# Kernel tuning notes

Hardware: AMD Instinct MI355X
Metric: run time of the kernel (lower is better)

The kernel has to match this reference:

```python
import jax, jax.numpy as jnp
import numpy as np

B, N, DIN, DH, H_MLP, L, C = 64, 1024, 64, 128, 128, 3, 4


def setup_inputs() -> dict:
    key = jax.random.key(0)
    ks = jax.random.split(key, 12)
    s = 0.05  # weight scale for numerical stability
    return {
        "x": jax.random.normal(ks[0], (B, N, DIN), jnp.float32),
        "U": jax.random.normal(ks[1], (3, N, N), jnp.float32) / np.sqrt(N),
        "w1_0": jax.random.normal(ks[2], (3, DIN, H_MLP), jnp.float32) * s,
        "b1_0": jnp.zeros((3, H_MLP), jnp.float32),
        "w2_0": jax.random.normal(ks[3], (3, H_MLP, DH), jnp.float32) * s,
        "b2_0": jnp.zeros((3, DH), jnp.float32),
        "w1_r": jax.random.normal(ks[4], (L - 1, 3, DH, H_MLP), jnp.float32) * s,
        "b1_r": jnp.zeros((L - 1, 3, H_MLP), jnp.float32),
        "w2_r": jax.random.normal(ks[5], (L - 1, 3, H_MLP, DH), jnp.float32) * s,
        "b2_r": jnp.zeros((L - 1, 3, DH), jnp.float32),
        "bw": jnp.ones((L, 3), jnp.float32),  # weight1/2/3 init to 1.0 per layer
        "Wc1": jax.random.normal(ks[6], (DH, 128), jnp.float32) * s,
        "bc1": jnp.zeros((128,), jnp.float32),
        "alpha": jnp.full((128,), 0.25, jnp.float32),  # PReLU init
        "Wc2": jax.random.normal(ks[7], (128, C), jnp.float32) * s,
        "bc2": jnp.zeros((C,), jnp.float32),
    }


def _gcn_multi(h, U, w1, b1, w2, b2, w3):
    """One GraphConv_multi layer: 3 spectral branches, softmax-weighted sum.
    h: [B,N,D_in], U: [3,N,N], w1:[3,Din,H], w2:[3,H,Dout], w3:[3]."""
    # agg = U^T @ h per branch (U is shared across batch; no repeat needed)
    agg = jnp.einsum('kji,bjd->kbid', U, h)                     # [3,B,N,Din]
    m = jax.nn.relu(jnp.einsum('kbid,kdh->kbih', agg, w1) + b1[:, None, None, :])
    m = jnp.einsum('kbih,kho->kbio', m, w2) + b2[:, None, None, :]  # [3,B,N,Dout]
    out = jnp.einsum('kij,kbjd->kbid', U, m)                    # U @ mlp_out
    ws = jax.nn.softmax(w3)                                     # branch mix
    return jnp.einsum('k,kbid->bid', ws, out)


def reference(x, U, w1_0, b1_0, w2_0, b2_0, w1_r, b1_r, w2_r, b2_r,
              bw, Wc1, bc1, alpha, Wc2, bc2):
    h = jax.nn.relu(_gcn_multi(x, U, w1_0, b1_0, w2_0, b2_0, bw[0]))
    for l in range(w1_r.shape[0]):  # remaining num_layers-1 GCN layers
        h = jax.nn.relu(_gcn_multi(h, U, w1_r[l], b1_r[l], w2_r[l], b2_r[l], bw[l + 1]))
    pooled = jnp.mean(h, axis=1)                                # 'mean' graph pooling
    z = pooled @ Wc1 + bc1
    z = jnp.where(z > 0, z, alpha * z)                          # PReLU(128); dropout = eval no-op
    return z @ Wc2 + bc2                                        # [B, C]
```

## Files before the change

### kernel.cpp

```cpp
#include <hip/hip_runtime.h>


typedef unsigned short u16;
typedef short bf16x8 __attribute__((ext_vector_type(8)));
typedef float f32x4 __attribute__((ext_vector_type(4)));
typedef u16 u16x4 __attribute__((ext_vector_type(4)));

__device__ __forceinline__ u16 f2bf(float x){
  unsigned u = __builtin_bit_cast(unsigned, x);
  u += 0x7fffu + ((u >> 16) & 1u);
  return (u16)(u >> 16);
}
__device__ __forceinline__ float bf2f(u16 h){
  return __builtin_bit_cast(float, ((unsigned)h) << 16);
}
__device__ __forceinline__ void gload16(const u16* g, u16* l){
  __builtin_amdgcn_global_load_lds(
      (const __attribute__((address_space(1))) unsigned int*)(g),
      (__attribute__((address_space(3))) unsigned int*)(l), 16, 0, 0);
}


__global__ void prep_weights(const float* __restrict__ w1_0, const float* __restrict__ w2_0,
                             const float* __restrict__ w1_r, const float* __restrict__ w2_r,
                             const float* __restrict__ bw,
                             u16* __restrict__ W1T0, u16* __restrict__ W2T0,
                             u16* __restrict__ W1Tr, u16* __restrict__ W2Tr,
                             float* __restrict__ wsb){
  int id = blockIdx.x*256 + threadIdx.x;
  if (id < 3){
    float a0=bw[id*3+0], a1=bw[id*3+1], a2=bw[id*3+2];
    float m = fmaxf(a0,fmaxf(a1,a2));
    float e0=expf(a0-m), e1=expf(a1-m), e2=expf(a2-m);
    float s = e0+e1+e2;
    wsb[id*3+0]=e0/s; wsb[id*3+1]=e1/s; wsb[id*3+2]=e2/s;
  }
  if (id < 24576){
    int k=id/8192, rem=id%8192, h=rem/64, d=rem%64;
    W1T0[id] = f2bf(w1_0[(k*64+d)*128 + h]);
  } else if (id < 73728){
    int t=id-24576, k=t/16384, rem=t%16384, o=rem/128, h=rem%128;
    W2T0[t] = f2bf(w2_0[(k*128+h)*128 + o]);
  } else if (id < 172032){
    int t=id-73728, lk=t/16384, rem=t%16384, h=rem/128, d=rem%128;
    W1Tr[t] = f2bf(w1_r[lk*16384 + d*128 + h]);
  } else if (id < 270336){
    int t=id-172032, lk=t/16384, rem=t%16384, o=rem/128, h=rem%128;
    W2Tr[t] = f2bf(w2_r[lk*16384 + h*128 + o]);
  }
}

__global__ void prep_U(const float* __restrict__ U, u16* __restrict__ UTcat,
                       u16* __restrict__ Ucat){
  __shared__ float t[32][33];
  int k = blockIdx.z, i0 = blockIdx.x*32, j0 = blockIdx.y*32;
  size_t kb = (size_t)k << 20;
  #pragma unroll
  for (int rr=0; rr<4; rr++){
    int r = threadIdx.y*4+rr, c = threadIdx.x;
    float v = U[kb + (size_t)(j0+r)*1024 + i0+c];
    t[r][c] = v;
    Ucat[(size_t)(j0+r)*3072 + k*1024 + i0+c] = f2bf(v);
  }
  __syncthreads();
  #pragma unroll
  for (int rr=0; rr<4; rr++){
    int r = threadIdx.y*4+rr, c = threadIdx.x;
    UTcat[kb + (size_t)(i0+r)*1024 + j0+c] = f2bf(t[c][r]);
  }
}

__global__ void prep_x(const float* __restrict__ x, u16* __restrict__ H){
  __shared__ float t[32][33];
  int b = blockIdx.z, d0 = blockIdx.x*32, j0 = blockIdx.y*32;
  #pragma unroll
  for (int rr=0;rr<4;rr++){
    int r=threadIdx.y*4+rr, c=threadIdx.x;
    t[r][c] = x[((size_t)b*1024 + j0+r)*64 + d0+c];
  }
  __syncthreads();
  #pragma unroll
  for (int rr=0;rr<4;rr++){
    int r=threadIdx.y*4+rr, c=threadIdx.x;
    H[(size_t)(b*64 + d0+r)*1024 + j0+c] = f2bf(t[c][r]);
  }
}

template<bool RELU, int REORD>
__global__ __launch_bounds__(512, 4)
void gemm_big(const u16* __restrict__ A, const u16* __restrict__ B,
              u16* __restrict__ C, int Nc, int K, long aZ, int cRowZ)
{
  __shared__ __align__(16) u16 ldsA[3*8192];
  __shared__ __align__(16) u16 ldsB[3*4096];
  const int tid = threadIdx.x;
  const int z = blockIdx.z;
  const u16* Ab = A + (size_t)z*aZ;
  const int gx = gridDim.x;
  const int nwg = gx*gridDim.y;
  int flat = blockIdx.y*gx + blockIdx.x;
  if ((nwg & 7) == 0) flat = (flat & 7)*(nwg >> 3) + (flat >> 3);
  const int bm = (flat/gx)*256, bn = (flat%gx)*128;
  const int wave = tid>>6, lane = tid&63;
  const int wm = (wave&3)*64, wn = (wave>>2)*64;
  const int rl = lane&15, ksb = lane>>4;
  const int srow = tid>>2;
  const int scol = ((tid&3)*8) ^ (((tid>>3)&3)<<3);
  const int NT = K>>5;

  f32x4 acc[4][4];
  #pragma unroll
  for (int mi=0;mi<4;mi++)
    #pragma unroll
    for (int ni=0;ni<4;ni++){ f32x4 zv={0.f,0.f,0.f,0.f}; acc[mi][ni]=zv; }

  auto stage = [&](int t){
    const int sa = (t%3)*8192, sb = (t%3)*4096;
    const int k0 = t<<5;
    #pragma unroll
    for (int c=0;c<2;c++)
      gload16(Ab + (size_t)(bm + c*128 + srow)*K + k0 + scol,
              &ldsA[sa + c*4096 + tid*8]);
    gload16(B + (size_t)(bn + srow)*K + k0 + scol, &ldsB[sb + tid*8]);
  };

  stage(0); stage(1);
  asm volatile("s_waitcnt vmcnt(3)" ::: "memory");
  __builtin_amdgcn_s_barrier();
  __builtin_amdgcn_sched_barrier(0);

  for (int t=0; t<NT; t++){
    const int sa = (t%3)*8192, sb = (t%3)*4096;
    bf16x8 af[4], bfr[4];
    #pragma unroll
    for (int mi=0;mi<4;mi++){
      const int row = wm + mi*16 + rl;
      af[mi] = *(const bf16x8*)&ldsA[sa + row*32 + ((ksb*8) ^ (((row>>1)&3)<<3))];
    }
    #pragma unroll
    for (int ni=0;ni<4;ni++){
      const int row = wn + ni*16 + rl;
      bfr[ni] = *(const bf16x8*)&ldsB[sb + row*32 + ((ksb*8) ^ (((row>>1)&3)<<3))];
    }
    if (t+2 < NT) stage(t+2);
    __builtin_amdgcn_s_setprio(1);
    #pragma unroll
    for (int ni=0;ni<4;ni++)
      #pragma unroll
      for (int mi=0;mi<4;mi++)
        acc[mi][ni] = __builtin_amdgcn_mfma_f32_16x16x32_bf16(af[mi], bfr[ni], acc[mi][ni], 0,0,0);
    __builtin_amdgcn_s_setprio(0);
    if (t+2 < NT)      asm volatile("s_waitcnt vmcnt(3)" ::: "memory");
    else if (t+1 < NT) asm volatile("s_waitcnt vmcnt(0)" ::: "memory");
    __builtin_amdgcn_s_barrier();
    __builtin_amdgcn_sched_barrier(0);
  }

  #pragma unroll
  for (int ni=0;ni<4;ni++){
    const int col = bn + wn + ni*16 + rl;
    #pragma unroll
    for (int mi=0;mi<4;mi++){
      const int row0 = bm + wm + mi*16 + ksb*4;
      #pragma unroll
      for (int r=0;r<4;r++){
        float v = acc[mi][ni][r];
        if (RELU) v = fmaxf(v, 0.f);
        if constexpr (REORD){
          const int Din = 1 << REORD;
          const int bb = col >> REORD, d = col & (Din-1);
          C[((size_t)((z<<6) + bb)*1024 + row0 + r)*Din + d] = f2bf(v);
        } else {
          C[(size_t)(z*cRowZ + row0 + r)*Nc + col] = f2bf(v);
        }
      }
    }
  }
}

__global__ __launch_bounds__(512, 2)
void gemm_agg_mlp(const u16* __restrict__ A, const u16* __restrict__ B,
                  const u16* __restrict__ W1T, const u16* __restrict__ W2T,
                  const float* __restrict__ b1g, const float* __restrict__ b2g,
                  const float* __restrict__ wsl, u16* __restrict__ M2T)
{
  __shared__ __align__(16) u16 lds[69632];
  const int tid = threadIdx.x;
  const int z = blockIdx.z;
  const int K = 1024, NT = 32;
  const u16* Ab = A + (size_t)z*1048576;
  const u16* W1k = W1T + z*16384;
  const u16* W2k = W2T + z*16384;
  const int gx = gridDim.x;
  const int nwg = gx*gridDim.y;
  int flat = blockIdx.y*gx + blockIdx.x;
  if ((nwg & 7) == 0) flat = (flat & 7)*(nwg >> 3) + (flat >> 3);
  const int bm = (flat/gx)*256, bn = (flat%gx)*128;
  const int b = bn >> 7;
  const int wave = tid>>6, lane = tid&63;
  const int wm = (wave&3)*64, wn = (wave>>2)*64;
  const int rl = lane&15, ksb = lane>>4;
  const int xr = (rl&7)<<3;
  const int srow = tid>>2;
  const int scol = ((tid&3)*8) ^ (((tid>>3)&3)<<3);

  f32x4 acc[4][4];
  #pragma unroll
  for (int mi=0;mi<4;mi++)
    #pragma unroll
    for (int ni=0;ni<4;ni++){ f32x4 zv={0.f,0.f,0.f,0.f}; acc[mi][ni]=zv; }

  #pragma unroll
  for (int c=0;c<4;c++){
    const int e = c*4096 + tid*8, row = e>>7, col = e&127;
    gload16(W1k + row*128 + (col ^ ((row&7)<<3)), &lds[36864 + e]);
  }
  #pragma unroll
  for (int c=0;c<4;c++){
    const int e = c*4096 + tid*8, row = e>>7, col = e&127;
    gload16(W2k + row*128 + (col ^ ((row&7)<<3)), &lds[53248 + e]);
  }

  auto stage = [&](int t){
    const int sa = (t%3)*8192, sb = 24576 + (t%3)*4096;
    const int k0 = t<<5;
    #pragma unroll
    for (int c=0;c<2;c++)
      gload16(Ab + (size_t)(bm + c*128 + srow)*K + k0 + scol,
              &lds[sa + c*4096 + tid*8]);
    gload16(B + (size_t)(bn + srow)*K + k0 + scol, &lds[sb + tid*8]);
  };

  stage(0); stage(1);
  asm volatile("s_waitcnt vmcnt(3)" ::: "memory");
  __builtin_amdgcn_s_barrier();
  __builtin_amdgcn_sched_barrier(0);

  for (int t=0; t<NT; t++){
    const int sa = (t%3)*8192, sb = 24576 + (t%3)*4096;
    bf16x8 af[4], bfr[4];
    #pragma unroll
    for (int mi=0;mi<4;mi++){
      const int row = wm + mi*16 + rl;
      af[mi] = *(const bf16x8*)&lds[sa + row*32 + ((ksb*8) ^ (((row>>1)&3)<<3))];
    }
    #pragma unroll
    for (int ni=0;ni<4;ni++){
      const int row = wn + ni*16 + rl;
      bfr[ni] = *(const bf16x8*)&lds[sb + row*32 + ((ksb*8) ^ (((row>>1)&3)<<3))];
    }
    if (t+2 < NT) stage(t+2);
    __builtin_amdgcn_s_setprio(1);
    #pragma unroll
    for (int ni=0;ni<4;ni++)
      #pragma unroll
      for (int mi=0;mi<4;mi++)
        acc[mi][ni] = __builtin_amdgcn_mfma_f32_16x16x32_bf16(af[mi], bfr[ni], acc[mi][ni], 0,0,0);
    __builtin_amdgcn_s_setprio(0);
    if (t+2 < NT)      asm volatile("s_waitcnt vmcnt(3)" ::: "memory");
    else if (t+1 < NT) asm volatile("s_waitcnt vmcnt(0)" ::: "memory");
    __builtin_amdgcn_s_barrier();
    __builtin_amdgcn_sched_barrier(0);
  }

  __syncthreads();
  #pragma unroll
  for (int ni=0;ni<4;ni++){
    const int d = wn + ni*16 + rl;
    #pragma unroll
    for (int mi=0;mi<4;mi++){
      #pragma unroll
      for (int r=0;r<4;r++){
        const int j = wm + mi*16 + ksb*4 + r;
        lds[j*128 + (d ^ ((j&7)<<3))] = f2bf(acc[mi][ni][r]);
      }
    }
  }
  __syncthreads();

  const int jg = (wave&3)*64, hg = (wave>>2)*64;
  f32x4 acc1[4][4];
  #pragma unroll
  for (int mi=0;mi<4;mi++)
    #pragma unroll
    for (int ni=0;ni<4;ni++){ f32x4 zv={0.f,0.f,0.f,0.f}; acc1[mi][ni]=zv; }
  #pragma unroll
  for (int kk=0;kk<4;kk++){
    const int k0 = kk*32;
    bf16x8 aj[4], wh[4];
    #pragma unroll
    for (int mi=0;mi<4;mi++)
      aj[mi] = *(const bf16x8*)&lds[(jg+mi*16+rl)*128 + ((k0+ksb*8) ^ xr)];
    #pragma unroll
    for (int ni=0;ni<4;ni++)
      wh[ni] = *(const bf16x8*)&lds[36864 + (hg+ni*16+rl)*128 + ((k0+ksb*8) ^ xr)];
    #pragma unroll
    for (int ni=0;ni<4;ni++)
      #pragma unroll
      for (int mi=0;mi<4;mi++)
        acc1[mi][ni] = __builtin_amdgcn_mfma_f32_16x16x32_bf16(aj[mi], wh[ni], acc1[mi][ni], 0,0,0);
  }
  __syncthreads();

  float bh[4];
  #pragma unroll
  for (int ni=0;ni<4;ni++) bh[ni] = b1g[z*128 + hg + ni*16 + rl];
  #pragma unroll
  for (int ni=0;ni<4;ni++){
    const int h = hg + ni*16 + rl;
    #pragma unroll
    for (int mi=0;mi<4;mi++){
      #pragma unroll
      for (int r=0;r<4;r++){
        const int j = jg + mi*16 + ksb*4 + r;
        lds[j*128 + (h ^ ((j&7)<<3))] = f2bf(fmaxf(acc1[mi][ni][r] + bh[ni], 0.f));
      }
    }
  }
  __syncthreads();

  const int og = (wave>>2)*64, jg2 = (wave&3)*64;
  f32x4 acc2[4][4];
  #pragma unroll
  for (int mi=0;mi<4;mi++)
    #pragma unroll
    for (int ni=0;ni<4;ni++){ f32x4 zv={0.f,0.f,0.f,0.f}; acc2[mi][ni]=zv; }
  #pragma unroll
  for (int kk=0;kk<4;kk++){
    const int k0 = kk*32;
    bf16x8 wo[4], mj[4];
    #pragma unroll
    for (int mi=0;mi<4;mi++)
      wo[mi] = *(const bf16x8*)&lds[53248 + (og+mi*16+rl)*128 + ((k0+ksb*8) ^ xr)];
    #pragma unroll
    for (int ni=0;ni<4;ni++)
      mj[ni] = *(const bf16x8*)&lds[(jg2+ni*16+rl)*128 + ((k0+ksb*8) ^ xr)];
    #pragma unroll
    for (int ni=0;ni<4;ni++)
      #pragma unroll
      for (int mi=0;mi<4;mi++)
        acc2[mi][ni] = __builtin_amdgcn_mfma_f32_16x16x32_bf16(wo[mi], mj[ni], acc2[mi][ni], 0,0,0);
  }

  const float ws = wsl[z];
  #pragma unroll
  for (int mi=0;mi<4;mi++){
    #pragma unroll
    for (int r=0;r<4;r++){
      const int o = og + mi*16 + ksb*4 + r;
      const float bo = b2g[z*128 + o];
      #pragma unroll
      for (int ni=0;ni<4;ni++){
        const int j = jg2 + ni*16 + rl;
        M2T[(size_t)(b*128 + o)*3072 + z*1024 + bm + j] = f2bf((acc2[mi][ni][r] + bo) * ws);
      }
    }
  }
}

template<int DIN>
__global__ __launch_bounds__(256)
void fused_mlp(const u16* __restrict__ AGG, const u16* __restrict__ W1T,
               const u16* __restrict__ W2T, const float* __restrict__ b1g,
               const float* __restrict__ b2g, const float* __restrict__ wsl,
               u16* __restrict__ M2T)
{
  constexpr int JW1 = 128*DIN;
  __shared__ __align__(16) u16 lds[2*JW1 + 16384];
  const int tid = threadIdx.x;
  const int jt = blockIdx.x, z = blockIdx.z, k = z>>6, b = z&63;
  const u16* Ag  = AGG + ((size_t)z*1024 + jt*128)*DIN;
  const u16* W1k = W1T + k*JW1;
  const u16* W2k = W2T + k*16384;
  const int wave = tid>>6, lane = tid&63;
  const int wm = (wave>>1)*64, wn = (wave&1)*64;
  const int rl = lane&15, ksb = lane>>4;
  const int xr = (rl&7)<<3;

  constexpr int CJ = JW1/2048;
  #pragma unroll
  for (int c=0;c<CJ;c++){
    const int e = c*2048 + tid*8, row = e/DIN, col = e%DIN;
    gload16(Ag + (size_t)row*DIN + (col ^ ((row&7)<<3)), &lds[e]);
  }
  #pragma unroll
  for (int c=0;c<CJ;c++){
    const int e = c*2048 + tid*8, row = e/DIN, col = e%DIN;
    gload16(W1k + (size_t)row*DIN + (col ^ ((row&7)<<3)), &lds[JW1 + e]);
  }
  #pragma unroll
  for (int c=0;c<8;c++){
    const int e = c*2048 + tid*8, row = e>>7, col = e&127;
    gload16(W2k + (size_t)row*128 + (col ^ ((row&7)<<3)), &lds[2*JW1 + e]);
  }
  asm volatile("s_waitcnt vmcnt(8)" ::: "memory");
  __builtin_amdgcn_s_barrier();
  __builtin_amdgcn_sched_barrier(0);

  f32x4 acc[4][4];
  #pragma unroll
  for (int mi=0;mi<4;mi++)
    #pragma unroll
    for (int ni=0;ni<4;ni++){ f32x4 zv={0.f,0.f,0.f,0.f}; acc[mi][ni]=zv; }
  #pragma unroll
  for (int k0=0; k0<DIN; k0+=32){
    bf16x8 aj[4], wh[4];
    #pragma unroll
    for (int mi=0;mi<4;mi++)
      aj[mi] = *(const bf16x8*)&lds[(wm+mi*16+rl)*DIN + ((k0+ksb*8) ^ xr)];
    #pragma unroll
    for (int ni=0;ni<4;ni++)
      wh[ni] = *(const bf16x8*)&lds[JW1 + (wn+ni*16+rl)*DIN + ((k0+ksb*8) ^ xr)];
    #pragma unroll
    for (int ni=0;ni<4;ni++)
      #pragma unroll
      for (int mi=0;mi<4;mi++)
        acc[mi][ni] = __builtin_amdgcn_mfma_f32_16x16x32_bf16(aj[mi], wh[ni], acc[mi][ni], 0,0,0);
  }
  __syncthreads();

  float bh[4];
  #pragma unroll
  for (int ni=0;ni<4;ni++) bh[ni] = b1g[k*128 + wn + ni*16 + rl];
  #pragma unroll
  for (int ni=0;ni<4;ni++){
    const int h = wn + ni*16 + rl;
    #pragma unroll
    for (int mi=0;mi<4;mi++){
      #pragma unroll
      for (int r=0;r<4;r++){
        const int j = wm + mi*16 + ksb*4 + r;
        lds[j*128 + (h ^ ((j&7)<<3))] = f2bf(fmaxf(acc[mi][ni][r] + bh[ni], 0.f));
      }
    }
  }
  __syncthreads();

  f32x4 acc2[4][4];
  #pragma unroll
  for (int mi=0;mi<4;mi++)
    #pragma unroll
    for (int ni=0;ni<4;ni++){ f32x4 zv={0.f,0.f,0.f,0.f}; acc2[mi][ni]=zv; }
  #pragma unroll
  for (int k0=0; k0<128; k0+=32){
    bf16x8 ao[4], mj[4];
    #pragma unroll
    for (int mi=0;mi<4;mi++)
      ao[mi] = *(const bf16x8*)&lds[2*JW1 + (wm+mi*16+rl)*128 + ((k0+ksb*8) ^ xr)];
    #pragma unroll
    for (int ni=0;ni<4;ni++)
      mj[ni] = *(const bf16x8*)&lds[(wn+ni*16+rl)*128 + ((k0+ksb*8) ^ xr)];
    #pragma unroll
    for (int ni=0;ni<4;ni++)
      #pragma unroll
      for (int mi=0;mi<4;mi++)
        acc2[mi][ni] = __builtin_amdgcn_mfma_f32_16x16x32_bf16(ao[mi], mj[ni], acc2[mi][ni], 0,0,0);
  }

  const float ws = wsl[k];
  #pragma unroll
  for (int mi=0;mi<4;mi++){
    #pragma unroll
    for (int r=0;r<4;r++){
      const int o = wm + mi*16 + ksb*4 + r;
      const float bo = b2g[k*128 + o];
      #pragma unroll
      for (int ni=0;ni<4;ni++){
        const int j = wn + ni*16 + rl;
        M2T[(size_t)(b*128 + o)*3072 + k*1024 + jt*128 + j] = f2bf((acc2[mi][ni][r] + bo) * ws);
      }
    }
  }
}

__global__ void pool_kernel(const u16* __restrict__ H, float* __restrict__ pooled){
  const int row = blockIdx.x, t = threadIdx.x;
  u16x4 v = *(const u16x4*)(H + (size_t)row*1024 + t*4);
  float s = bf2f(v.x)+bf2f(v.y)+bf2f(v.z)+bf2f(v.w);
  for (int o2=32;o2>0;o2>>=1) s += __shfl_down(s,o2);
  __shared__ float red[4];
  if ((t&63)==0) red[t>>6]=s;
  __syncthreads();
  if (t==0) pooled[row] = (red[0]+red[1]+red[2]+red[3])*(1.f/1024.f);
}

__global__ void head_kernel(const float* __restrict__ pooled, const float* __restrict__ Wc1,
                            const float* __restrict__ bc1, const float* __restrict__ alpha,
                            const float* __restrict__ Wc2, const float* __restrict__ bc2,
                            float* __restrict__ out){
  const int b = blockIdx.x, h = threadIdx.x;
  __shared__ float p[128], zz[128];
  p[h] = pooled[b*128+h];
  __syncthreads();
  float acc = bc1[h];
  for (int d=0; d<128; d++) acc = fmaf(p[d], Wc1[d*128+h], acc);
  zz[h] = acc>0.f ? acc : alpha[h]*acc;
  __syncthreads();
  if (h<4){
    float a = bc2[h];
    for (int q=0;q<128;q++) a = fmaf(zz[q], Wc2[q*4+h], a);
    out[b*4+h]=a;
  }
}

extern "C" void kernel_launch(void* const* d_in, const int* in_sizes, int n_in,
                              void* d_out, int out_size, void* d_ws, size_t ws_size,
                              hipStream_t stream)
{
  const float* x     = (const float*)d_in[0];
  const float* U     = (const float*)d_in[1];
  const float* w1_0  = (const float*)d_in[2];
  const float* b1_0  = (const float*)d_in[3];
  const float* w2_0  = (const float*)d_in[4];
  const float* b2_0  = (const float*)d_in[5];
  const float* w1_r  = (const float*)d_in[6];
  const float* b1_r  = (const float*)d_in[7];
  const float* w2_r  = (const float*)d_in[8];
  const float* b2_r  = (const float*)d_in[9];
  const float* bw    = (const float*)d_in[10];
  const float* Wc1   = (const float*)d_in[11];
  const float* bc1   = (const float*)d_in[12];
  const float* alpha = (const float*)d_in[13];
  const float* Wc2   = (const float*)d_in[14];
  const float* bc2   = (const float*)d_in[15];
  float* out = (float*)d_out;

  char* wsp = (char*)d_ws;
  size_t off = 0;
  auto alloc = [&](size_t bytes) -> void* {
    void* p = wsp + off;
    off = (off + bytes + 255) & ~(size_t)255;
    return p;
  };
  u16* UTcat = (u16*)alloc(6291456);
  u16* Ucat  = (u16*)alloc(6291456);
  u16* W1T0  = (u16*)alloc(49152);
  u16* W2T0  = (u16*)alloc(98304);
  u16* W1Tr  = (u16*)alloc(196608);
  u16* W2Tr  = (u16*)alloc(196608);
  float* wsb = (float*)alloc(256);
  u16* HT    = (u16*)alloc(16777216);
  u16* AGG   = (u16*)alloc(50331648);
  u16* M2T   = (u16*)alloc(50331648);
  float* pooled = (float*)alloc(32768);
  if (off > ws_size) return;

  prep_weights<<<1056, 256, 0, stream>>>(w1_0,w2_0,w1_r,w2_r,bw,
      W1T0,W2T0,W1Tr,W2Tr,wsb);
  prep_U<<<dim3(32,32,3), dim3(32,8), 0, stream>>>(U, UTcat, Ucat);
  prep_x<<<dim3(2,32,64), dim3(32,8), 0, stream>>>(x, HT);

  for (int l=0; l<3; l++){
    const float* b1 = l ? b1_r + (l-1)*384 : b1_0;
    const float* b2 = l ? b2_r + (l-1)*384 : b2_0;

    if (l == 0){
      gemm_big<false,6><<<dim3(32, 4, 3), 512, 0, stream>>>(
          UTcat, HT, AGG, 4096, 1024, 1048576L, 0);
      fused_mlp<64><<<dim3(8, 1, 192), 256, 0, stream>>>(
          AGG, W1T0, W2T0, b1, b2, wsb, M2T);
    } else {
      gemm_agg_mlp<<<dim3(64, 4, 3), 512, 0, stream>>>(
          UTcat, HT,
          W1Tr + (size_t)(l-1)*3*16384, W2Tr + (size_t)(l-1)*3*16384,
          b1, b2, wsb + l*3, M2T);
    }
    gemm_big<true,0><<<dim3(8, 32, 1), 512, 0, stream>>>(
        M2T, Ucat, HT, 1024, 3072, 0L, 0);
  }
  pool_kernel<<<8192, 256, 0, stream>>>(HT, pooled);
  head_kernel<<<64, 128, 0, stream>>>(pooled, Wc1, bc1, alpha, Wc2, bc2, out);
}
```

Before: 413.0 us.

## Fuse mean pooling into final GEMM epilogue and shrink agg-MLP LDS footprint

The last layer's U@M GEMM now reduces its ReLU outputs per row into partial sums instead of writing the full bf16 activation tensor. A small combine kernel then sums the 16 partials into the pooled vector, which removes a 16 MB write plus reread and the separate pool pass. Separately, gemm_agg_mlp stops staging W1/W2 in LDS and reads them straight from global memory. It processes the MLP in four 64-row chunks, cutting LDS use so launch bounds can request 4 blocks per CU instead of 2. The tradeoff is more global or L2 weight traffic and extra barriers per chunk.

```diff
diff --git a/kernel.cpp b/kernel.cpp
--- a/kernel.cpp
+++ b/kernel.cpp
@@ -86,10 +86,11 @@
   }
 }
 
-template<bool RELU, int REORD>
+template<bool RELU, int REORD, bool POOL>
 __global__ __launch_bounds__(512, 4)
 void gemm_big(const u16* __restrict__ A, const u16* __restrict__ B,
-              u16* __restrict__ C, int Nc, int K, long aZ, int cRowZ)
+              u16* __restrict__ C, float* __restrict__ Pp,
+              int Nc, int K, long aZ, int cRowZ)
 {
   __shared__ __align__(16) u16 ldsA[3*8192];
   __shared__ __align__(16) u16 ldsB[3*4096];
@@ -156,6 +157,26 @@
     __builtin_amdgcn_sched_barrier(0);
   }
 
+  if constexpr (POOL){
+    const int bx = flat % gx;
+    #pragma unroll
+    for (int mi=0;mi<4;mi++){
+      #pragma unroll
+      for (int r=0;r<4;r++){
+        float s = 0.f;
+        #pragma unroll
+        for (int ni=0;ni<4;ni++) s += fmaxf(acc[mi][ni][r], 0.f);
+        s += __shfl_xor(s, 1); s += __shfl_xor(s, 2);
+        s += __shfl_xor(s, 4); s += __shfl_xor(s, 8);
+        if ((lane & 15) == 0){
+          const int row = bm + wm + mi*16 + ksb*4 + r;
+          Pp[(size_t)(bx*2 + (wn>>6))*8192 + row] = s;
+        }
+      }
+    }
+    return;
+  }
+
   #pragma unroll
   for (int ni=0;ni<4;ni++){
     const int col = bn + wn + ni*16 + rl;
@@ -178,13 +199,13 @@
   }
 }
 
-__global__ __launch_bounds__(512, 2)
+__global__ __launch_bounds__(512, 4)
 void gemm_agg_mlp(const u16* __restrict__ A, const u16* __restrict__ B,
                   const u16* __restrict__ W1T, const u16* __restrict__ W2T,
                   const float* __restrict__ b1g, const float* __restrict__ b2g,
                   const float* __restrict__ wsl, u16* __restrict__ M2T)
 {
-  __shared__ __align__(16) u16 lds[69632];
+  __shared__ __align__(16) u16 lds[40960];
   const int tid = threadIdx.x;
   const int z = blockIdx.z;
   const int K = 1024, NT = 32;
@@ -210,17 +231,6 @@
     #pragma unroll
     for (int ni=0;ni<4;ni++){ f32x4 zv={0.f,0.f,0.f,0.f}; acc[mi][ni]=zv; }
 
-  #pragma unroll
-  for (int c=0;c<4;c++){
-    const int e = c*4096 + tid*8, row = e>>7, col = e&127;
-    gload16(W1k + row*128 + (col ^ ((row&7)<<3)), &lds[36864 + e]);
-  }
-  #pragma unroll
-  for (int c=0;c<4;c++){
-    const int e = c*4096 + tid*8, row = e>>7, col = e&127;
-    gload16(W2k + row*128 + (col ^ ((row&7)<<3)), &lds[53248 + e]);
-  }
-
   auto stage = [&](int t){
     const int sa = (t%3)*8192, sb = 24576 + (t%3)*4096;
     const int k0 = t<<5;
@@ -278,83 +288,70 @@
   }
   __syncthreads();
 
-  const int jg = (wave&3)*64, hg = (wave>>2)*64;
-  f32x4 acc1[4][4];
-  #pragma unroll
-  for (int mi=0;mi<4;mi++)
-    #pragma unroll
-    for (int ni=0;ni<4;ni++){ f32x4 zv={0.f,0.f,0.f,0.f}; acc1[mi][ni]=zv; }
-  #pragma unroll
-  for (int kk=0;kk<4;kk++){
-    const int k0 = kk*32;
-    bf16x8 aj[4], wh[4];
-    #pragma unroll
-    for (int mi=0;mi<4;mi++)
-      aj[mi] = *(const bf16x8*)&lds[(jg+mi*16+rl)*128 + ((k0+ksb*8) ^ xr)];
-    #pragma unroll
-    for (int ni=0;ni<4;ni++)
-      wh[ni] = *(const bf16x8*)&lds[36864 + (hg+ni*16+rl)*128 + ((k0+ksb*8) ^ xr)];
-    #pragma unroll
-    for (int ni=0;ni<4;ni++)
-      #pragma unroll
-      for (int mi=0;mi<4;mi++)
-        acc1[mi][ni] = __builtin_amdgcn_mfma_f32_16x16x32_bf16(aj[mi], wh[ni], acc1[mi][ni], 0,0,0);
-  }
-  __syncthreads();
-
-  float bh[4];
-  #pragma unroll
-  for (int ni=0;ni<4;ni++) bh[ni] = b1g[z*128 + hg + ni*16 + rl];
-  #pragma unroll
-  for (int ni=0;ni<4;ni++){
-    const int h = hg + ni*16 + rl;
+  const float ws = wsl[z];
+  for (int p=0; p<4; p++){
+    const int hg = wave*16;
+    const int h  = hg + rl;
+    const float bh = b1g[z*128 + h];
+    f32x4 acc1[4];
+    #pragma unroll
+    for (int mi=0;mi<4;mi++){ f32x4 zv={0.f,0.f,0.f,0.f}; acc1[mi]=zv; }
+    #pragma unroll
+    for (int kk=0;kk<4;kk++){
+      const int k0 = kk*32;
+      const bf16x8 wh = *(const bf16x8*)(W1k + (size_t)h*128 + k0 + ksb*8);
+      #pragma unroll
+      for (int mi=0;mi<4;mi++){
+        const bf16x8 aj = *(const bf16x8*)&lds[(p*64+mi*16+rl)*128 + ((k0+ksb*8) ^ xr)];
+        acc1[mi] = __builtin_amdgcn_mfma_f32_16x16x32_bf16(aj, wh, acc1[mi], 0,0,0);
+      }
+    }
     #pragma unroll
     for (int mi=0;mi<4;mi++){
       #pragma unroll
       for (int r=0;r<4;r++){
-        const int j = jg + mi*16 + ksb*4 + r;
-        lds[j*128 + (h ^ ((j&7)<<3))] = f2bf(fmaxf(acc1[mi][ni][r] + bh[ni], 0.f));
-      }
-    }
-  }
-  __syncthreads();
-
-  const int og = (wave>>2)*64, jg2 = (wave&3)*64;
-  f32x4 acc2[4][4];
-  #pragma unroll
-  for (int mi=0;mi<4;mi++)
-    #pragma unroll
-    for (int ni=0;ni<4;ni++){ f32x4 zv={0.f,0.f,0.f,0.f}; acc2[mi][ni]=zv; }
-  #pragma unroll
-  for (int kk=0;kk<4;kk++){
-    const int k0 = kk*32;
-    bf16x8 wo[4], mj[4];
-    #pragma unroll
-    for (int mi=0;mi<4;mi++)
-      wo[mi] = *(const bf16x8*)&lds[53248 + (og+mi*16+rl)*128 + ((k0+ksb*8) ^ xr)];
-    #pragma unroll
-    for (int ni=0;ni<4;ni++)
-      mj[ni] = *(const bf16x8*)&lds[(jg2+ni*16+rl)*128 + ((k0+ksb*8) ^ xr)];
-    #pragma unroll
-    for (int ni=0;ni<4;ni++)
-      #pragma unroll
-      for (int mi=0;mi<4;mi++)
-        acc2[mi][ni] = __builtin_amdgcn_mfma_f32_16x16x32_bf16(wo[mi], mj[ni], acc2[mi][ni], 0,0,0);
-  }
-
-  const float ws = wsl[z];
-  #pragma unroll
-  for (int mi=0;mi<4;mi++){
-    #pragma unroll
-    for (int r=0;r<4;r++){
-      const int o = og + mi*16 + ksb*4 + r;
-      const float bo = b2g[z*128 + o];
-      #pragma unroll
-      for (int ni=0;ni<4;ni++){
-        const int j = jg2 + ni*16 + rl;
-        M2T[(size_t)(b*128 + o)*3072 + z*1024 + bm + j] = f2bf((acc2[mi][ni][r] + bo) * ws);
-      }
-    }
+        const int jl = mi*16 + ksb*4 + r;
+        lds[32768 + jl*128 + (h ^ ((jl&7)<<3))] = f2bf(fmaxf(acc1[mi][r] + bh, 0.f));
+      }
+    }
+    __syncthreads();
+    const int og = (wave>>1)*32, jg2 = (wave&1)*32;
+    f32x4 acc2[2][2];
+    #pragma unroll
+    for (int mi=0;mi<2;mi++)
+      #pragma unroll
+      for (int ni=0;ni<2;ni++){ f32x4 zv={0.f,0.f,0.f,0.f}; acc2[mi][ni]=zv; }
+    #pragma unroll
+    for (int kk=0;kk<4;kk++){
+      const int k0 = kk*32;
+      bf16x8 wo[2], mj[2];
+      #pragma unroll
+      for (int mi=0;mi<2;mi++)
+        wo[mi] = *(const bf16x8*)(W2k + (size_t)(og+mi*16+rl)*128 + k0 + ksb*8);
+      #pragma unroll
+      for (int ni=0;ni<2;ni++)
+        mj[ni] = *(const bf16x8*)&lds[32768 + (jg2+ni*16+rl)*128 + ((k0+ksb*8) ^ xr)];
+      #pragma unroll
+      for (int ni=0;ni<2;ni++)
+        #pragma unroll
+        for (int mi=0;mi<2;mi++)
+          acc2[mi][ni] = __builtin_amdgcn_mfma_f32_16x16x32_bf16(wo[mi], mj[ni], acc2[mi][ni], 0,0,0);
+    }
+    #pragma unroll
+    for (int mi=0;mi<2;mi++){
+      #pragma unroll
+      for (int r=0;r<4;r++){
+        const int o = og + mi*16 + ksb*4 + r;
+        const float bo = b2g[z*128 + o];
+        #pragma unroll
+        for (int ni=0;ni<2;ni++){
+          const int jl = jg2 + ni*16 + rl;
+          M2T[(size_t)(b*128 + o)*3072 + z*1024 + bm + p*64 + jl]
+              = f2bf((acc2[mi][ni][r] + bo) * ws);
+        }
+      }
+    }
+    __syncthreads();
   }
 }
 
@@ -473,15 +470,12 @@
   }
 }
 
-__global__ void pool_kernel(const u16* __restrict__ H, float* __restrict__ pooled){
-  const int row = blockIdx.x, t = threadIdx.x;
-  u16x4 v = *(const u16x4*)(H + (size_t)row*1024 + t*4);
-  float s = bf2f(v.x)+bf2f(v.y)+bf2f(v.z)+bf2f(v.w);
-  for (int o2=32;o2>0;o2>>=1) s += __shfl_down(s,o2);
-  __shared__ float red[4];
-  if ((t&63)==0) red[t>>6]=s;
-  __syncthreads();
-  if (t==0) pooled[row] = (red[0]+red[1]+red[2]+red[3])*(1.f/1024.f);
+__global__ void pool_combine(const float* __restrict__ Pp, float* __restrict__ pooled){
+  const int row = blockIdx.x*256 + threadIdx.x;
+  float s = 0.f;
+  #pragma unroll
+  for (int i=0;i<16;i++) s += Pp[(size_t)i*8192 + row];
+  pooled[row] = s * (1.f/1024.f);
 }
 
 __global__ void head_kernel(const float* __restrict__ pooled, const float* __restrict__ Wc1,
@@ -542,7 +536,8 @@
   u16* HT    = (u16*)alloc(16777216);
   u16* AGG   = (u16*)alloc(50331648);
   u16* M2T   = (u16*)alloc(50331648);
-  float* pooled = (float*)alloc(32768);
+  float* partials = (float*)alloc(524288);
+  float* pooled   = (float*)alloc(32768);
   if (off > ws_size) return;
 
   prep_weights<<<1056, 256, 0, stream>>>(w1_0,w2_0,w1_r,w2_r,bw,
@@ -555,8 +550,8 @@
     const float* b2 = l ? b2_r + (l-1)*384 : b2_0;
 
     if (l == 0){
-      gemm_big<false,6><<<dim3(32, 4, 3), 512, 0, stream>>>(
-          UTcat, HT, AGG, 4096, 1024, 1048576L, 0);
+      gemm_big<false,6,false><<<dim3(32, 4, 3), 512, 0, stream>>>(
+          UTcat, HT, AGG, nullptr, 4096, 1024, 1048576L, 0);
       fused_mlp<64><<<dim3(8, 1, 192), 256, 0, stream>>>(
           AGG, W1T0, W2T0, b1, b2, wsb, M2T);
     } else {
@@ -565,9 +560,13 @@
           W1Tr + (size_t)(l-1)*3*16384, W2Tr + (size_t)(l-1)*3*16384,
           b1, b2, wsb + l*3, M2T);
     }
-    gemm_big<true,0><<<dim3(8, 32, 1), 512, 0, stream>>>(
-        M2T, Ucat, HT, 1024, 3072, 0L, 0);
-  }
-  pool_kernel<<<8192, 256, 0, stream>>>(HT, pooled);
+    if (l < 2)
+      gemm_big<true,0,false><<<dim3(8, 32, 1), 512, 0, stream>>>(
+          M2T, Ucat, HT, nullptr, 1024, 3072, 0L, 0);
+    else
+      gemm_big<true,0,true><<<dim3(8, 32, 1), 512, 0, stream>>>(
+          M2T, Ucat, nullptr, partials, 1024, 3072, 0L, 0);
+  }
+  pool_combine<<<32, 256, 0, stream>>>(partials, pooled);
   head_kernel<<<64, 128, 0, stream>>>(pooled, Wc1, bc1, alpha, Wc2, bc2, out);
 }
```

Result: no change. 408.8 us (-1.0%).
